# Kernel tuning notes

Measured on AMD Instinct MI355X. Metric: run time of the kernel, lower is better.

## Reference

```python
import jax, jax.numpy as jnp
import numpy as np

HEADS = 8
DIM_HEAD_KQ = 8
DIM_HEAD_V = 16
DIM = 128
IN_CH = 128
QKV_CH = DIM_HEAD_V + 2 * DIM_HEAD_KQ  # 32
OUT_CH = HEADS * QKV_CH               # 256
EPS = 1e-5


def setup_inputs() -> dict:
    key = jax.random.key(0)
    ks = jax.random.split(key, 7)
    b = 2048  # batch * width
    return {
        "x_in": jax.random.normal(ks[0], (b, IN_CH, DIM), jnp.float32),
        "conv_w": jax.random.normal(ks[1], (OUT_CH, IN_CH), jnp.float32) * (IN_CH ** -0.5),
        "bn_gamma": 1.0 + 0.1 * jax.random.normal(ks[2], (OUT_CH,), jnp.float32),
        "bn_beta": 0.1 * jax.random.normal(ks[3], (OUT_CH,), jnp.float32),
        "bn_mean": 0.1 * jax.random.normal(ks[4], (OUT_CH,), jnp.float32),
        "bn_var": jax.random.uniform(ks[5], (OUT_CH,), jnp.float32, 0.5, 1.5),
        "relative": jax.random.normal(ks[6], (QKV_CH, 2 * DIM - 1), jnp.float32),
    }


def reference(x_in, conv_w, bn_gamma, bn_beta, bn_mean, bn_var, relative):
    scale = DIM ** -0.5
    b = x_in.shape[0]

    # 1x1 conv + BatchNorm1d (inference mode, running stats)
    y = jnp.einsum('bcd,oc->bod', x_in, conv_w)  # [b, 256, DIM]
    inv = bn_gamma / jnp.sqrt(bn_var + EPS)
    y = (y - bn_mean[:, None]) * inv[:, None] + bn_beta[:, None]

    # rearrange 'b (q h) d -> b h q d' with q=QKV_CH, h=HEADS
    qkv = y.reshape(b, QKV_CH, HEADS, DIM).transpose(0, 2, 1, 3)  # [b,h,32,DIM]
    q = qkv[:, :, :DIM_HEAD_KQ] * scale           # [b,h,8,DIM]
    k = qkv[:, :, DIM_HEAD_KQ:2 * DIM_HEAD_KQ]    # [b,h,8,DIM]
    v = qkv[:, :, 2 * DIM_HEAD_KQ:]               # [b,h,16,DIM]

    # relative position gather: all_emb[c, a, j] = relative[c, a - j + DIM - 1]
    idx = jnp.arange(DIM)
    rel_idx = idx[:, None] - idx[None, :] + DIM - 1  # [DIM, DIM]
    all_emb = relative[:, rel_idx]                   # [32, DIM, DIM]
    q_emb = all_emb[:DIM_HEAD_KQ]
    k_emb = all_emb[DIM_HEAD_KQ:2 * DIM_HEAD_KQ]
    v_emb = all_emb[2 * DIM_HEAD_KQ:]

    qr = jnp.einsum('bhid,idj->bhdj', q, q_emb)      # [b,h,DIM,DIM]
    kr = jnp.einsum('bhid,idj->bhdj', k, k_emb)
    dots = jnp.einsum('bhid,bhij->bhdj', q, k)
    attn = jax.nn.softmax(qr + kr + dots, axis=-1)

    out = jnp.einsum('bhdj,bhij->bhid', attn, v)     # [b,h,16,DIM]
    kv = jnp.einsum('bhdj,idj->bhid', attn, v_emb)   # [b,h,16,DIM]

    # rearrange 'b h i d -> b (h i) d'
    return (kv + out).reshape(b, HEADS * DIM_HEAD_V, DIM)
```

## Files before the change

### kernel.cpp

```cpp
#include <hip/hip_runtime.h>

typedef __attribute__((ext_vector_type(8))) short short8;
typedef __attribute__((ext_vector_type(4))) short short4v;
typedef __attribute__((ext_vector_type(4))) float float4v;
typedef unsigned short ushort_t;
typedef __bf16 bf16_t;

#define MFMA16(A,B,C) __builtin_amdgcn_mfma_f32_16x16x32_bf16((A),(B),(C),0,0,0)
#define LOG2E 1.4426950408889634f

#define OFF_EQKH 0
#define OFF_EQKL 8192
#define OFF_QH   16384
#define OFF_QL   22528
#define OFF_ATT  0
#define OFF_EVV  36864
#define OFF_IB   49664
#define LDS_BYTES 49920

__device__ __forceinline__ ushort_t f2bf(float f) {
  return __builtin_bit_cast(ushort_t, (bf16_t)f);
}
__device__ __forceinline__ float bf2f(ushort_t s) {
  return __builtin_bit_cast(float, ((unsigned)s) << 16);
}
__device__ __forceinline__ short8 ld8_2x4(const char* p) {
  short4v a = *(const short4v*)p;
  short4v b = *(const short4v*)(p + 8);
  return (short8){a[0],a[1],a[2],a[3],b[0],b[1],b[2],b[3]};
}
__device__ __forceinline__ short8 sel8(bool c, short8 a) {
  short8 r;
  #pragma unroll
  for (int k = 0; k < 8; ++k) r[k] = c ? a[k] : (short)0;
  return r;
}

__global__ __launch_bounds__(512, 6) void axial_fused(
    const float* __restrict__ xg,
    const float* __restrict__ wg,
    const float* __restrict__ gg, const float* __restrict__ btg,
    const float* __restrict__ mng, const float* __restrict__ vrg,
    const float* __restrict__ relg,
    float* __restrict__ outg)
{
  __shared__ __align__(64) char L[LDS_BYTES];
  const int tid  = threadIdx.x;
  const unsigned bid = blockIdx.x;
  const int xcd = bid & 7;
  const unsigned li = bid >> 3;
  const int h = (int)(li & 7);
  const int b = (int)((li >> 3) * 8 + (unsigned)xcd);
  const int w    = tid >> 6;
  const int lane = tid & 63;
  const int q    = lane >> 4;
  const int m16  = lane & 15;
  const int qbase = lane & 48;

  #pragma unroll
  for (int e0 = 0; e0 < 4096; e0 += 512) {
    int e = e0 + tid;
    int i = e >> 8, t = e & 255;
    float r1 = 0.f, r2 = 0.f;
    if (t < 255) { int m = 254 - t; r1 = relg[i * 255 + m] * LOG2E; r2 = relg[(16 + i) * 255 + m]; }
    ushort_t h1 = f2bf(r1);
    *(ushort_t*)(L + OFF_EQKH + t * 32 + i * 2) = h1;
    *(ushort_t*)(L + OFF_EQKL + t * 32 + i * 2) = f2bf(r1 - bf2f(h1));
    *(ushort_t*)(L + OFF_EVV + i * 800 + t * 2) = f2bf(r2);
  }
  if (tid < 256) {
    int i = tid >> 4, t = 256 + (tid & 15);
    *(ushort_t*)(L + OFF_EVV + i * 800 + t * 2) = 0;
  }
  if (tid < 32) {
    int og = tid * 8 + h;
    float inv = gg[og] / sqrtf(vrg[og] + 1e-5f);
    ((float*)(L + OFF_IB))[tid * 2]     = inv;
    ((float*)(L + OFF_IB))[tid * 2 + 1] = btg[og] - mng[og] * inv;
  }
  __syncthreads();

  {
    const int d = w * 16 + m16;
    const float* xb = xg + (size_t)b * 16384 + d;
    const int og0 = m16 * 8 + h;
    float4v acc0 = {0,0,0,0}, acc1 = {0,0,0,0};
    #pragma unroll
    for (int cc = 0; cc < 4; ++cc) {
      const int cb = cc * 32;
      short8 xh, xl;
      #pragma unroll
      for (int jj = 0; jj < 8; ++jj) {
        float xv = xb[(cb + q * 8 + jj) * 128];
        ushort_t hh = f2bf(xv);
        xh[jj] = (short)hh; xl[jj] = (short)f2bf(xv - bf2f(hh));
      }
      const float* wp0 = wg + og0 * 128 + cb + q * 8;
      const float* wp1 = wp0 + 16384;
      short8 wh0, wl0, wh1, wl1;
      #pragma unroll
      for (int jj = 0; jj < 8; ++jj) {
        float f0 = wp0[jj]; ushort_t h0 = f2bf(f0);
        wh0[jj] = (short)h0; wl0[jj] = (short)f2bf(f0 - bf2f(h0));
        float f1 = wp1[jj]; ushort_t h1 = f2bf(f1);
        wh1[jj] = (short)h1; wl1[jj] = (short)f2bf(f1 - bf2f(h1));
      }
      acc0 = MFMA16(wh0, xh, acc0);
      acc0 = MFMA16(wl0, xh, acc0);
      acc0 = MFMA16(wh0, xl, acc0);
      acc1 = MFMA16(wh1, xh, acc1);
      acc1 = MFMA16(wl1, xh, acc1);
      acc1 = MFMA16(wh1, xl, acc1);
    }
    const float* ib = (const float*)(L + OFF_IB);
    {
      const float sc = (q < 2) ? 0.08838834764831845f : 1.0f;
      short4v hi4, lo4, kt4;
      #pragma unroll
      for (int r = 0; r < 4; ++r) {
        int o = q * 4 + r;
        float y = (acc0[r] * ib[o * 2] + ib[o * 2 + 1]) * sc;
        ushort_t hh = f2bf(y);
        hi4[r] = (short)hh; lo4[r] = (short)f2bf(y - bf2f(hh));
        kt4[r] = (short)f2bf(y * LOG2E);
      }
      *(short4v*)(L + OFF_QH + d * 48 + q * 8) = hi4;
      *(short4v*)(L + OFF_QL + d * 40 + q * 8) = lo4;
      if (q >= 2) *(short4v*)(L + OFF_QH + d * 48 + 32 + (q - 2) * 8) = kt4;
    }
    #pragma unroll
    for (int r = 0; r < 4; ++r) {
      int o = 16 + q * 4 + r;
      float y = acc1[r] * ib[o * 2] + ib[o * 2 + 1];
      *(ushort_t*)(L + OFF_EVV + (q * 4 + r) * 800 + 544 + d * 2) = f2bf(y);
    }
  }
  __syncthreads();

  const int toff = 112 - w * 16;
  const int rowd = w * 16 + m16;
  short8 A1 = *(const short8*)(L + OFF_QH + rowd * 48 + (q & 1) * 16);
  short8 A2 = sel8(q < 2, ld8_2x4(L + OFF_QL + rowd * 40 + (q & 1) * 16));
  float4v sc[9];
  {
    const char* eb = L + ((q < 2) ? OFF_EQKH : OFF_EQKL) + (q & 1) * 16;
    #pragma unroll
    for (int tk = 0; tk < 9; ++tk) {
      short8 b1 = *(const short8*)(eb + (tk * 16 + m16 + toff) * 32);
      float4v z = {0,0,0,0};
      float4v c = MFMA16(A1, b1, z);
      sc[tk] = MFMA16(A2, b1, c);
    }
  }
  {
    short8 Ad = sel8(q == 0, A1);
    const int base0 = m16 + q * 4 + 1;
    #pragma unroll
    for (int jt = 0; jt < 8; ++jt) {
      short8 bk = sel8(q == 0, *(const short8*)(L + OFF_QH + (jt * 16 + m16) * 48 + 32));
      float4v z = {0,0,0,0};
      float4v c = MFMA16(Ad, bk, z);
      #pragma unroll
      for (int r = 0; r < 4; ++r) {
        int u = base0 + r;
        int sl = (u & 15) | qbase;
        float rot = __shfl(c[r], sl, 64);
        bool ge = (u & 16) != 0;
        sc[jt][r]     += ge ? rot : 0.0f;
        sc[jt + 1][r] += ge ? 0.0f : rot;
      }
    }
    #pragma unroll
    for (int r = 0; r < 4; ++r) {
      bool ge = ((base0 + r) & 16) != 0;
      sc[0][r] = ge ? sc[0][r] : -1e30f;
      sc[8][r] = ge ? -1e30f : sc[8][r];
    }
  }
  __syncthreads();

  float rs[4];
  {
    #pragma unroll
    for (int r = 0; r < 4; ++r) {
      float mx = sc[0][r];
      #pragma unroll
      for (int tk = 1; tk < 9; ++tk) mx = fmaxf(mx, sc[tk][r]);
      #pragma unroll
      for (int off = 1; off <= 8; off <<= 1) mx = fmaxf(mx, __shfl_xor(mx, off, 64));
      float e[9]; float s = 0.f;
      #pragma unroll
      for (int tk = 0; tk < 9; ++tk) { e[tk] = __builtin_exp2f(sc[tk][r] - mx); s += e[tk]; }
      #pragma unroll
      for (int off = 1; off <= 8; off <<= 1) s += __shfl_xor(s, off, 64);
      rs[r] = 1.0f / s;
      const int dd = w * 16 + q * 4 + r;
      const size_t rowp = (size_t)(L + OFF_ATT) + (size_t)dd * 288;
      const size_t sw = ((dd >> 2) & 3) << 4;
      #pragma unroll
      for (int tk = 0; tk < 9; ++tk)
        *(ushort_t*)((rowp + (tk * 16 + m16) * 2) ^ sw) = f2bf(e[tk]);
    }
  }
  __syncthreads();

  {
    float4v acc = {0,0,0,0};
    const char* evrow = L + OFF_EVV + m16 * 800;
    const size_t abase = (size_t)(L + OFF_ATT) + (size_t)rowd * 288;
    const size_t swz = ((rowd >> 2) & 3) << 4;
    #pragma unroll
    for (int kk = 0; kk < 4; ++kk) {
      short8 af;
      #pragma unroll
      for (int jj = 0; jj < 8; ++jj) {
        int ttg = kk * 32 + q * 8 + jj + 15 - m16;
        af[jj] = *(const short*)((abase + ttg * 2) ^ swz);
      }
      short8 bf = *(const short8*)(evrow + 544 + (kk * 32 + q * 8) * 2);
      acc = MFMA16(af, bf, acc);
    }
    #pragma unroll
    for (int kk = 0; kk < 5; ++kk) {
      short8 af;
      if (kk == 4 && q >= 2) af = (short8){0,0,0,0,0,0,0,0};
      else af = *(const short8*)((abase + (kk * 32 + q * 8) * 2) ^ swz);
      short8 bf = *(const short8*)(evrow + (toff + kk * 32 + q * 8) * 2);
      acc = MFMA16(af, bf, acc);
    }
    #pragma unroll
    for (int r = 0; r < 4; ++r) acc[r] *= rs[r];
    float* op = outg + (size_t)b * 16384 + (h * 16 + m16) * 128 + w * 16 + q * 4;
    *(float4v*)op = acc;
  }
}

extern "C" void kernel_launch(void* const* d_in, const int* in_sizes, int n_in,
                              void* d_out, int out_size, void* d_ws, size_t ws_size,
                              hipStream_t stream) {
  const float* xg   = (const float*)d_in[0];
  const float* wg   = (const float*)d_in[1];
  const float* gg   = (const float*)d_in[2];
  const float* btg  = (const float*)d_in[3];
  const float* mng  = (const float*)d_in[4];
  const float* vrg  = (const float*)d_in[5];
  const float* relg = (const float*)d_in[6];
  float* outg = (float*)d_out;
  axial_fused<<<dim3(16384), dim3(512), 0, stream>>>(xg, wg, gg, btg, mng, vrg, relg, outg);
}
```

Measured before the change: 596.2 us.

## Precompute relative embeddings in a prep kernel and stage conv weights through LDS

Adds a small prep kernel that converts the relative-position table into bf16 hi/lo layouts in workspace once per call, so each block copies them with vectorized float4 loads instead of gathering and converting 8K scalars. Conv weights for the head are split into bf16 hi/lo once per block into LDS, replacing per-lane redundant global loads and conversions. LDS layouts are repadded (stride 40 and 272) and an extra barrier is added; the q==0 masking on one operand is dropped since the other operand is already masked. This costs an extra kernel launch and slightly more LDS.

```diff
diff --git a/kernel.cpp b/kernel.cpp
--- a/kernel.cpp
+++ b/kernel.cpp
@@ -9,14 +9,19 @@
 #define MFMA16(A,B,C) __builtin_amdgcn_mfma_f32_16x16x32_bf16((A),(B),(C),0,0,0)
 #define LOG2E 1.4426950408889634f
 
+#define WS_BYTES 29440
+
 #define OFF_EQKH 0
-#define OFF_EQKL 8192
-#define OFF_QH   16384
-#define OFF_QL   22528
+#define OFF_EQKL 10240
+#define OFF_WH   20480
+#define OFF_WL   29184
+#define OFF_QH   20480
+#define OFF_QL   26624
 #define OFF_ATT  0
-#define OFF_EVV  36864
-#define OFF_IB   49664
-#define LDS_BYTES 49920
+#define OFF_EVR  37888
+#define OFF_V    46848
+#define OFF_IB   51200
+#define LDS_BYTES 51456
 
 __device__ __forceinline__ ushort_t f2bf(float f) {
   return __builtin_bit_cast(ushort_t, (bf16_t)f);
@@ -36,12 +41,31 @@
   return r;
 }
 
+__global__ __launch_bounds__(512) void prep_rel(const float* __restrict__ relg,
+                                                char* __restrict__ ws) {
+  int idx = blockIdx.x * 512 + threadIdx.x;
+  if (idx < 4096) {
+    int i = idx & 15, t = idx >> 4;
+    float r1 = 0.f;
+    if (t < 255) r1 = relg[i * 255 + (254 - t)] * LOG2E;
+    ushort_t h1 = f2bf(r1);
+    *(ushort_t*)(ws + t * 40 + i * 2)         = h1;
+    *(ushort_t*)(ws + 10240 + t * 40 + i * 2) = f2bf(r1 - bf2f(h1));
+  } else if (idx < 8576) {
+    int k = idx - 4096;
+    int i = k / 280, c = k - i * 280;
+    float r2 = 0.f;
+    if (c < 255) r2 = relg[(16 + i) * 255 + (254 - c)];
+    *(ushort_t*)(ws + 20480 + i * 560 + c * 2) = f2bf(r2);
+  }
+}
+
 __global__ __launch_bounds__(512, 6) void axial_fused(
     const float* __restrict__ xg,
     const float* __restrict__ wg,
     const float* __restrict__ gg, const float* __restrict__ btg,
     const float* __restrict__ mng, const float* __restrict__ vrg,
-    const float* __restrict__ relg,
+    const char* __restrict__ wsg,
     float* __restrict__ outg)
 {
   __shared__ __align__(64) char L[LDS_BYTES];
@@ -58,19 +82,29 @@
   const int qbase = lane & 48;
 
   #pragma unroll
-  for (int e0 = 0; e0 < 4096; e0 += 512) {
-    int e = e0 + tid;
-    int i = e >> 8, t = e & 255;
-    float r1 = 0.f, r2 = 0.f;
-    if (t < 255) { int m = 254 - t; r1 = relg[i * 255 + m] * LOG2E; r2 = relg[(16 + i) * 255 + m]; }
-    ushort_t h1 = f2bf(r1);
-    *(ushort_t*)(L + OFF_EQKH + t * 32 + i * 2) = h1;
-    *(ushort_t*)(L + OFF_EQKL + t * 32 + i * 2) = f2bf(r1 - bf2f(h1));
-    *(ushort_t*)(L + OFF_EVV + i * 800 + t * 2) = f2bf(r2);
-  }
-  if (tid < 256) {
-    int i = tid >> 4, t = 256 + (tid & 15);
-    *(ushort_t*)(L + OFF_EVV + i * 800 + t * 2) = 0;
+  for (int u0 = 0; u0 < 1280; u0 += 512) {
+    int u = u0 + tid;
+    if (u < 1280) *(float4v*)(L + u * 16) = *(const float4v*)(wsg + u * 16);
+  }
+  {
+    *(float4v*)(L + OFF_EVR + tid * 16) = *(const float4v*)(wsg + 20480 + tid * 16);
+    if (tid < 48) {
+      int u2 = 512 + tid;
+      *(float4v*)(L + OFF_EVR + u2 * 16) = *(const float4v*)(wsg + 20480 + u2 * 16);
+    }
+  }
+  {
+    int o = tid >> 4, c0 = (tid & 15) * 8;
+    const float* wrow = wg + (o * 8 + h) * 128 + c0;
+    short8 hi, lo;
+    #pragma unroll
+    for (int k = 0; k < 8; ++k) {
+      float f = wrow[k];
+      ushort_t hh = f2bf(f);
+      hi[k] = (short)hh; lo[k] = (short)f2bf(f - bf2f(hh));
+    }
+    *(short8*)(L + OFF_WH + o * 272 + c0 * 2) = hi;
+    *(short8*)(L + OFF_WL + o * 272 + c0 * 2) = lo;
   }
   if (tid < 32) {
     int og = tid * 8 + h;
@@ -80,11 +114,10 @@
   }
   __syncthreads();
 
+  float4v acc0 = {0,0,0,0}, acc1 = {0,0,0,0};
   {
     const int d = w * 16 + m16;
     const float* xb = xg + (size_t)b * 16384 + d;
-    const int og0 = m16 * 8 + h;
-    float4v acc0 = {0,0,0,0}, acc1 = {0,0,0,0};
     #pragma unroll
     for (int cc = 0; cc < 4; ++cc) {
       const int cb = cc * 32;
@@ -95,16 +128,12 @@
         ushort_t hh = f2bf(xv);
         xh[jj] = (short)hh; xl[jj] = (short)f2bf(xv - bf2f(hh));
       }
-      const float* wp0 = wg + og0 * 128 + cb + q * 8;
-      const float* wp1 = wp0 + 16384;
-      short8 wh0, wl0, wh1, wl1;
-      #pragma unroll
-      for (int jj = 0; jj < 8; ++jj) {
-        float f0 = wp0[jj]; ushort_t h0 = f2bf(f0);
-        wh0[jj] = (short)h0; wl0[jj] = (short)f2bf(f0 - bf2f(h0));
-        float f1 = wp1[jj]; ushort_t h1 = f2bf(f1);
-        wh1[jj] = (short)h1; wl1[jj] = (short)f2bf(f1 - bf2f(h1));
-      }
+      const char* wbh = L + OFF_WH + m16 * 272 + (cb + q * 8) * 2;
+      const char* wbl = L + OFF_WL + m16 * 272 + (cb + q * 8) * 2;
+      short8 wh0 = *(const short8*)(wbh);
+      short8 wh1 = *(const short8*)(wbh + 16 * 272);
+      short8 wl0 = *(const short8*)(wbl);
+      short8 wl1 = *(const short8*)(wbl + 16 * 272);
       acc0 = MFMA16(wh0, xh, acc0);
       acc0 = MFMA16(wl0, xh, acc0);
       acc0 = MFMA16(wh0, xl, acc0);
@@ -112,6 +141,11 @@
       acc1 = MFMA16(wl1, xh, acc1);
       acc1 = MFMA16(wh1, xl, acc1);
     }
+  }
+  __syncthreads();
+
+  {
+    const int d = w * 16 + m16;
     const float* ib = (const float*)(L + OFF_IB);
     {
       const float sc = (q < 2) ? 0.08838834764831845f : 1.0f;
@@ -132,7 +166,7 @@
     for (int r = 0; r < 4; ++r) {
       int o = 16 + q * 4 + r;
       float y = acc1[r] * ib[o * 2] + ib[o * 2 + 1];
-      *(ushort_t*)(L + OFF_EVV + (q * 4 + r) * 800 + 544 + d * 2) = f2bf(y);
+      *(ushort_t*)(L + OFF_V + (q * 4 + r) * 272 + d * 2) = f2bf(y);
     }
   }
   __syncthreads();
@@ -146,7 +180,7 @@
     const char* eb = L + ((q < 2) ? OFF_EQKH : OFF_EQKL) + (q & 1) * 16;
     #pragma unroll
     for (int tk = 0; tk < 9; ++tk) {
-      short8 b1 = *(const short8*)(eb + (tk * 16 + m16 + toff) * 32);
+      short8 b1 = ld8_2x4(eb + (tk * 16 + m16 + toff) * 40);
       float4v z = {0,0,0,0};
       float4v c = MFMA16(A1, b1, z);
       sc[tk] = MFMA16(A2, b1, c);
@@ -157,7 +191,7 @@
     const int base0 = m16 + q * 4 + 1;
     #pragma unroll
     for (int jt = 0; jt < 8; ++jt) {
-      short8 bk = sel8(q == 0, *(const short8*)(L + OFF_QH + (jt * 16 + m16) * 48 + 32));
+      short8 bk = *(const short8*)(L + OFF_QH + (jt * 16 + m16) * 48 + 32);
       float4v z = {0,0,0,0};
       float4v c = MFMA16(Ad, bk, z);
       #pragma unroll
@@ -206,7 +240,8 @@
 
   {
     float4v acc = {0,0,0,0};
-    const char* evrow = L + OFF_EVV + m16 * 800;
+    const char* evrow = L + OFF_EVR + m16 * 560;
+    const char* vrow  = L + OFF_V + m16 * 272;
     const size_t abase = (size_t)(L + OFF_ATT) + (size_t)rowd * 288;
     const size_t swz = ((rowd >> 2) & 3) << 4;
     #pragma unroll
@@ -217,7 +252,7 @@
         int ttg = kk * 32 + q * 8 + jj + 15 - m16;
         af[jj] = *(const short*)((abase + ttg * 2) ^ swz);
       }
-      short8 bf = *(const short8*)(evrow + 544 + (kk * 32 + q * 8) * 2);
+      short8 bf = *(const short8*)(vrow + (kk * 32 + q * 8) * 2);
       acc = MFMA16(af, bf, acc);
     }
     #pragma unroll
@@ -246,5 +281,7 @@
   const float* vrg  = (const float*)d_in[5];
   const float* relg = (const float*)d_in[6];
   float* outg = (float*)d_out;
-  axial_fused<<<dim3(16384), dim3(512), 0, stream>>>(xg, wg, gg, btg, mng, vrg, relg, outg);
-}
+  char* ws = (char*)d_ws;
+  prep_rel<<<dim3(17), dim3(512), 0, stream>>>(relg, ws);
+  axial_fused<<<dim3(16384), dim3(512), 0, stream>>>(xg, wg, gg, btg, mng, vrg, ws, outg);
+}
```

Result: faster. 487.1 us (-18.3%).
